# Kernel optimization log

Hardware: AMD Instinct MI355X
Metric: run time of the kernel (lower is better)

## Reference

```python
import jax, jax.numpy as jnp
import numpy as np

D_MODEL = 512
N_HEADS = 8
B, T = 2, 2048
EPS = 1e-6


def _phi(x):
    # ELU feature map: elu(x) + 1 (always positive)
    return jax.nn.elu(x) + 1.0


def setup_inputs() -> dict:
    key = jax.random.key(0)
    ks = jax.random.split(key, 9)
    s = 1.0 / np.sqrt(D_MODEL)
    x = jax.random.normal(ks[0], (B, T, D_MODEL), dtype=jnp.float32)
    Wq = jax.random.uniform(ks[1], (D_MODEL, D_MODEL), jnp.float32, -s, s)
    bq = jax.random.uniform(ks[2], (D_MODEL,), jnp.float32, -s, s)
    Wk = jax.random.uniform(ks[3], (D_MODEL, D_MODEL), jnp.float32, -s, s)
    bk = jax.random.uniform(ks[4], (D_MODEL,), jnp.float32, -s, s)
    Wv = jax.random.uniform(ks[5], (D_MODEL, D_MODEL), jnp.float32, -s, s)
    bv = jax.random.uniform(ks[6], (D_MODEL,), jnp.float32, -s, s)
    Wo = jax.random.uniform(ks[7], (D_MODEL, D_MODEL), jnp.float32, -s, s)
    bo = jax.random.uniform(ks[8], (D_MODEL,), jnp.float32, -s, s)
    return {"x": x, "Wq": Wq, "bq": bq, "Wk": Wk, "bk": bk,
            "Wv": Wv, "bv": bv, "Wo": Wo, "bo": bo}


def reference(x, Wq, bq, Wk, bk, Wv, bv, Wo, bo):
    Bb, Tt, _ = x.shape
    H = N_HEADS
    D = D_MODEL // H

    def heads(W, b):
        # (B,T,d_model) -> (B,H,T,D)
        return (x @ W + b).reshape(Bb, Tt, H, D).transpose(0, 2, 1, 3)

    Q = _phi(heads(Wq, bq))
    K = _phi(heads(Wk, bk))
    V = heads(Wv, bv)

    # Causal linear attention: S_t = sum_{j<=t} phi(K_j) ⊗ V_j, z_t = sum_{j<=t} phi(K_j)
    KV = jnp.einsum('bhtd,bhtm->bhtdm', K, V)   # (B,H,T,D,D)
    S = jnp.cumsum(KV, axis=2)
    z = jnp.cumsum(K, axis=2)
    num = jnp.einsum('bhtd,bhtdm->bhtm', Q, S)  # (B,H,T,D)
    den = jnp.maximum(jnp.einsum('bhtd,bhtd->bht', Q, z), EPS)[..., None]
    out = num / den

    out = out.transpose(0, 2, 1, 3).reshape(Bb, Tt, D_MODEL)
    return out @ Wo + bo
```

## Files before the change

### kernel.cpp

```cpp
#include <hip/hip_runtime.h>
#include <math.h>

#define DM 512
#define NH 8
#define HD 64
#define BB 2
#define TT 2048
#define CHUNK 64
#define NC (TT / CHUNK)
#define BH (BB * NH)
#define ROWS (BB * TT)
#define EPSV 1e-6f

typedef short bf16x8 __attribute__((ext_vector_type(8)));
typedef float f32x4 __attribute__((ext_vector_type(4)));
typedef unsigned short us;

union U4 { us h[4]; uint2 u; };

__device__ __forceinline__ us f2bf(float f) {
    unsigned int u = __float_as_uint(f);
    return (us)((u + 0x7FFFu + ((u >> 16) & 1u)) >> 16);
}
__device__ __forceinline__ float bf2f(us h) {
    return __uint_as_float(((unsigned int)h) << 16);
}
__device__ __forceinline__ void gload16(const void* g, void* l) {
    __builtin_amdgcn_global_load_lds(
        (const __attribute__((address_space(1))) unsigned int*)g,
        (__attribute__((address_space(3))) unsigned int*)l, 16, 0, 0);
}
#define SWZ(r, k) ((k) ^ (((r) & 7) << 3))

__global__ __launch_bounds__(256) void prep(
    const float* __restrict__ x,
    const float* __restrict__ Wq, const float* __restrict__ Wk,
    const float* __restrict__ Wv, const float* __restrict__ Wo,
    us* __restrict__ xb, us* __restrict__ WT)
{
    const int bid = blockIdx.x, tid = threadIdx.x;
    __shared__ float tl[32][33];
    if (bid < 2048) {
        const int i = bid * 256 + tid;
        float4 v = ((const float4*)x)[i];
        U4 o;
        o.h[0] = f2bf(v.x); o.h[1] = f2bf(v.y);
        o.h[2] = f2bf(v.z); o.h[3] = f2bf(v.w);
        ((uint2*)xb)[i] = o.u;
    } else {
        const int b2 = bid - 2048;
        const int which = b2 >> 8, t = b2 & 255;
        const float* W = (which == 0) ? Wq : (which == 1) ? Wk : (which == 2) ? Wv : Wo;
        us* O = WT + (size_t)which * DM * DM;
        const int r0 = (t >> 4) * 32, c0 = (t & 15) * 32;
        const int tr = tid >> 3, tc = tid & 7;
        float4 v = *(const float4*)&W[(size_t)(r0 + tr) * DM + c0 + tc * 4];
        tl[tr][tc * 4 + 0] = v.x; tl[tr][tc * 4 + 1] = v.y;
        tl[tr][tc * 4 + 2] = v.z; tl[tr][tc * 4 + 3] = v.w;
        __syncthreads();
        U4 o;
#pragma unroll
        for (int i = 0; i < 4; ++i) o.h[i] = f2bf(tl[tc * 4 + i][tr]);
        *(uint2*)&O[(size_t)(c0 + tr) * DM + r0 + tc * 4] = o.u;
    }
}

__device__ __forceinline__ void gemm64x128(
    const us* __restrict__ Ag, const us* __restrict__ Bg,
    int r0, int c0, int tid, us* Asl, us* Bsl, f32x4 (&acc)[2][4])
{
    const int lane = tid & 63, wid = tid >> 6;
    const int wr = wid >> 1, wc = wid & 1;
    const int lrow = lane & 15, lk8 = (lane >> 4) * 8;
    const int fa = tid * 8;

    for (int k0 = 0; k0 < DM; k0 += 64) {
        __syncthreads();
#pragma unroll
        for (int i = 0; i < 2; ++i) {
            const int f = fa + i * 2048, row = f >> 6, kp = f & 63;
            gload16(Ag + (size_t)(r0 + row) * DM + k0 + SWZ(row, kp), Asl + f);
        }
#pragma unroll
        for (int i = 0; i < 4; ++i) {
            const int f = fa + i * 2048, row = f >> 6, kp = f & 63;
            gload16(Bg + (size_t)(c0 + row) * DM + k0 + SWZ(row, kp), Bsl + f);
        }
        __syncthreads();
#pragma unroll
        for (int kin = 0; kin < 64; kin += 32) {
            bf16x8 af[2], bfr[4];
#pragma unroll
            for (int mi = 0; mi < 2; ++mi) {
                const int row = wr * 32 + mi * 16 + lrow;
                af[mi] = *(const bf16x8*)&Asl[row * 64 + SWZ(row, kin + lk8)];
            }
#pragma unroll
            for (int ni = 0; ni < 4; ++ni) {
                const int row = wc * 64 + ni * 16 + lrow;
                bfr[ni] = *(const bf16x8*)&Bsl[row * 64 + SWZ(row, kin + lk8)];
            }
#pragma unroll
            for (int mi = 0; mi < 2; ++mi)
#pragma unroll
                for (int ni = 0; ni < 4; ++ni)
                    acc[mi][ni] = __builtin_amdgcn_mfma_f32_16x16x32_bf16(
                        af[mi], bfr[ni], acc[mi][ni], 0, 0, 0);
        }
    }
}

__global__ __launch_bounds__(256) void qkv_mfma(
    const us* __restrict__ xb, const us* __restrict__ WT,
    const float* __restrict__ bq, const float* __restrict__ bk,
    const float* __restrict__ bv,
    us* __restrict__ qn, us* __restrict__ kn,
    us* __restrict__ kt, us* __restrict__ vt)
{
    const int which = blockIdx.z;
    const us* Bg = WT + (size_t)which * DM * DM;
    const float* bias = (which == 0) ? bq : (which == 1) ? bk : bv;

    __shared__ us Asl[64 * 64];
    __shared__ us Bsl[128 * 64];
    f32x4 acc[2][4] = {};
    const int r0 = blockIdx.x * 64, c0 = blockIdx.y * 128;
    const int tid = threadIdx.x;

    gemm64x128(xb, Bg, r0, c0, tid, Asl, Bsl, acc);

    const int lane = tid & 63, wid = tid >> 6;
    const int wr = wid >> 1, wc = wid & 1;
    const int lrow = lane & 15, lr4 = (lane >> 4) * 4;
    const int b = r0 >> 11;

#pragma unroll
    for (int mi = 0; mi < 2; ++mi) {
        const int rowb = r0 + wr * 32 + mi * 16 + lr4;
        const int t0g = rowb & (TT - 1);
#pragma unroll
        for (int ni = 0; ni < 4; ++ni) {
            const int col = c0 + wc * 64 + ni * 16 + lrow;
            const int h = col >> 6, d = col & 63;
            const float bc = bias[col];
            U4 p4;
#pragma unroll
            for (int r = 0; r < 4; ++r) {
                float y = acc[mi][ni][r] + bc;
                if (which < 2) y = (y > 0.f) ? (y + 1.f) : __expf(y);
                const us hb = f2bf(y);
                p4.h[r] = hb;
                if (which == 0)
                    qn[((size_t)(b * NH + h) * TT + t0g + r) * HD + d] = hb;
                else if (which == 1)
                    kn[((size_t)(b * NH + h) * TT + t0g + r) * HD + d] = hb;
            }
            if (which == 1)
                *(uint2*)&kt[((size_t)(b * NH + h) * HD + d) * TT + t0g] = p4.u;
            else if (which == 2)
                *(uint2*)&vt[((size_t)(b * NH + h) * HD + d) * TT + t0g] = p4.u;
        }
    }
}

__global__ __launch_bounds__(256) void out_mfma(
    const us* __restrict__ Ag, const us* __restrict__ WoT,
    const float* __restrict__ bias, float* __restrict__ out)
{
    __shared__ us Asl[64 * 64];
    __shared__ us Bsl[128 * 64];
    f32x4 acc[2][4] = {};
    const int r0 = blockIdx.x * 64, c0 = blockIdx.y * 128;
    const int tid = threadIdx.x;

    gemm64x128(Ag, WoT, r0, c0, tid, Asl, Bsl, acc);

    const int lane = tid & 63, wid = tid >> 6;
    const int wr = wid >> 1, wc = wid & 1;
    const int lrow = lane & 15, lr4 = (lane >> 4) * 4;

#pragma unroll
    for (int mi = 0; mi < 2; ++mi)
#pragma unroll
        for (int ni = 0; ni < 4; ++ni) {
            const int col = c0 + wc * 64 + ni * 16 + lrow;
            const float bc = bias[col];
#pragma unroll
            for (int r = 0; r < 4; ++r) {
                const int row = r0 + wr * 32 + mi * 16 + lr4 + r;
                out[(size_t)row * DM + col] = acc[mi][ni][r] + bc;
            }
        }
}

__global__ __launch_bounds__(256) void chunk_sums(
    const us* __restrict__ kt, const us* __restrict__ vt,
    us* __restrict__ kvc, float* __restrict__ zc)
{
    const int blk = blockIdx.x, bh = blk >> 5, c = blk & 31;
    const int t0 = c * CHUNK;
    __shared__ us Ksl[4096], Vsl[4096];
    __shared__ float partial[4][64];
    const int tid = threadIdx.x;
    const us* ktb = kt + (size_t)bh * HD * TT;
    const us* vtb = vt + (size_t)bh * HD * TT;

#pragma unroll
    for (int i = 0; i < 2; ++i) {
        const int f = tid * 8 + i * 2048, row = f >> 6, kp = f & 63;
        const int kl = SWZ(row, kp);
        gload16(ktb + (size_t)row * TT + t0 + kl, Ksl + f);
        gload16(vtb + (size_t)row * TT + t0 + kl, Vsl + f);
    }
    __syncthreads();

    const int lane = tid & 63, wid = tid >> 6;
    const int wr = wid >> 1, wc = wid & 1;
    const int lrow = lane & 15, lk8 = (lane >> 4) * 8, lr4 = (lane >> 4) * 4;

    f32x4 acc[2][2] = {};
#pragma unroll
    for (int kin = 0; kin < 64; kin += 32) {
        bf16x8 af[2], bfr[2];
#pragma unroll
        for (int mi = 0; mi < 2; ++mi) {
            const int row = wr * 32 + mi * 16 + lrow;
            af[mi] = *(const bf16x8*)&Vsl[row * 64 + SWZ(row, kin + lk8)];
        }
#pragma unroll
        for (int ni = 0; ni < 2; ++ni) {
            const int row = wc * 32 + ni * 16 + lrow;
            bfr[ni] = *(const bf16x8*)&Ksl[row * 64 + SWZ(row, kin + lk8)];
        }
#pragma unroll
        for (int mi = 0; mi < 2; ++mi)
#pragma unroll
            for (int ni = 0; ni < 2; ++ni)
                acc[mi][ni] = __builtin_amdgcn_mfma_f32_16x16x32_bf16(
                    af[mi], bfr[ni], acc[mi][ni], 0, 0, 0);
    }

    us* dst = kvc + (size_t)blk * 4096;
#pragma unroll
    for (int mi = 0; mi < 2; ++mi)
#pragma unroll
        for (int ni = 0; ni < 2; ++ni) {
            const int d2 = wr * 32 + mi * 16 + lr4;
            const int d1 = wc * 32 + ni * 16 + lrow;
#pragma unroll
            for (int r = 0; r < 4; ++r)
                dst[(d2 + r) * 64 + d1] = f2bf(acc[mi][ni][r]);
        }

    {
        const int p = tid >> 6, d = tid & 63;
        float s = 0.f;
#pragma unroll
        for (int j = 0; j < 16; ++j)
            s += bf2f(Ksl[d * 64 + SWZ(d, p * 16 + j)]);
        partial[p][d] = s;
    }
    __syncthreads();
    if (tid < 64)
        zc[(size_t)blk * 64 + tid] =
            partial[0][tid] + partial[1][tid] + partial[2][tid] + partial[3][tid];
}

__global__ __launch_bounds__(256) void scan(
    const us* __restrict__ kvc, const float* __restrict__ zc,
    us* __restrict__ spr, float* __restrict__ zpr)
{
    const int bh = blockIdx.x, seg = blockIdx.y, tid = threadIdx.x;
    if (seg < 8) {
        const int e = seg * 512 + tid * 2;
        float r0 = 0.f, r1 = 0.f;
        for (int c = 0; c < NC; ++c) {
            const size_t off = (size_t)(bh * NC + c) * 4096 + e;
            const unsigned u = *(const unsigned*)(kvc + off);
            const unsigned p = (unsigned)f2bf(r0) | ((unsigned)f2bf(r1) << 16);
            *(unsigned*)(spr + off) = p;
            r0 += bf2f((us)(u & 0xFFFF));
            r1 += bf2f((us)(u >> 16));
        }
    } else if (tid < 64) {
        float run = 0.f;
        for (int c = 0; c < NC; ++c) {
            const size_t off = (size_t)(bh * NC + c) * 64 + tid;
            zpr[off] = run;
            run += zc[off];
        }
    }
}

__global__ __launch_bounds__(256) void chunk_attn(
    const us* __restrict__ qn, const us* __restrict__ kn,
    const us* __restrict__ vt, const us* __restrict__ spr,
    const float* __restrict__ zpr, us* __restrict__ attn)
{
    const int blk = blockIdx.x, bh = blk >> 5, c = blk & 31;
    const int t0 = c * CHUNK;
    __shared__ us Qs[4096], Kns[4096], Vts[4096], Sts[4096], Abf[4096];
    __shared__ float zp[64], den[64], part[4][64];
    const int tid = threadIdx.x;

    const us* qb = qn + ((size_t)bh * TT + t0) * HD;
    const us* kb = kn + ((size_t)bh * TT + t0) * HD;
    const us* vb = vt + (size_t)bh * HD * TT;
    const us* sb = spr + (size_t)blk * 4096;

#pragma unroll
    for (int i = 0; i < 2; ++i) {
        const int f = tid * 8 + i * 2048, row = f >> 6, kp = f & 63;
        const int kl = SWZ(row, kp);
        gload16(qb + (size_t)row * HD + kl, Qs + f);
        gload16(kb + (size_t)row * HD + kl, Kns + f);
        gload16(vb + (size_t)row * TT + t0 + kl, Vts + f);
        gload16(sb + (size_t)row * 64 + kl, Sts + f);
    }
    if (tid < 64) zp[tid] = zpr[(size_t)blk * 64 + tid];
    __syncthreads();

    const int lane = tid & 63, wid = tid >> 6;
    const int wr = wid >> 1, wc = wid & 1;
    const int lrow = lane & 15, lk8 = (lane >> 4) * 8, lr4 = (lane >> 4) * 4;

    f32x4 accs[2][2] = {};
#pragma unroll
    for (int kin = 0; kin < 64; kin += 32) {
        bf16x8 af[2], bfr[2];
#pragma unroll
        for (int mi = 0; mi < 2; ++mi) {
            const int row = wr * 32 + mi * 16 + lrow;
            af[mi] = *(const bf16x8*)&Qs[row * 64 + SWZ(row, kin + lk8)];
        }
#pragma unroll
        for (int ni = 0; ni < 2; ++ni) {
            const int row = wc * 32 + ni * 16 + lrow;
            bfr[ni] = *(const bf16x8*)&Kns[row * 64 + SWZ(row, kin + lk8)];
        }
#pragma unroll
        for (int mi = 0; mi < 2; ++mi)
#pragma unroll
            for (int ni = 0; ni < 2; ++ni)
                accs[mi][ni] = __builtin_amdgcn_mfma_f32_16x16x32_bf16(
                    af[mi], bfr[ni], accs[mi][ni], 0, 0, 0);
    }

#pragma unroll
    for (int mi = 0; mi < 2; ++mi)
#pragma unroll
        for (int ni = 0; ni < 2; ++ni) {
            const int j = wc * 32 + ni * 16 + lrow;
#pragma unroll
            for (int r = 0; r < 4; ++r) {
                const int i = wr * 32 + mi * 16 + lr4 + r;
                const float v = (j <= i) ? accs[mi][ni][r] : 0.f;
                Abf[i * 64 + SWZ(i, j)] = f2bf(v);
            }
        }
    __syncthreads();

    {
        const int p = tid >> 6, i = tid & 63;
        float s = 0.f;
#pragma unroll
        for (int jj = 0; jj < 16; ++jj) {
            const int j = p * 16 + jj;
            s += bf2f(Abf[i * 64 + SWZ(i, j)]);
            s += bf2f(Qs[i * 64 + SWZ(i, j)]) * zp[j];
        }
        part[p][i] = s;
    }
    __syncthreads();
    if (tid < 64)
        den[tid] = fmaxf(part[0][tid] + part[1][tid] + part[2][tid] + part[3][tid], EPSV);
    __syncthreads();

    f32x4 acco[2][2] = {};
#pragma unroll
    for (int kin = 0; kin < 64; kin += 32) {
        bf16x8 af[2], bfr[2], ag[2], bgr[2];
#pragma unroll
        for (int mi = 0; mi < 2; ++mi) {
            const int row = wr * 32 + mi * 16 + lrow;
            af[mi] = *(const bf16x8*)&Abf[row * 64 + SWZ(row, kin + lk8)];
            ag[mi] = *(const bf16x8*)&Qs[row * 64 + SWZ(row, kin + lk8)];
        }
#pragma unroll
        for (int ni = 0; ni < 2; ++ni) {
            const int row = wc * 32 + ni * 16 + lrow;
            bfr[ni] = *(const bf16x8*)&Vts[row * 64 + SWZ(row, kin + lk8)];
            bgr[ni] = *(const bf16x8*)&Sts[row * 64 + SWZ(row, kin + lk8)];
        }
#pragma unroll
        for (int mi = 0; mi < 2; ++mi)
#pragma unroll
            for (int ni = 0; ni < 2; ++ni) {
                acco[mi][ni] = __builtin_amdgcn_mfma_f32_16x16x32_bf16(
                    af[mi], bfr[ni], acco[mi][ni], 0, 0, 0);
                acco[mi][ni] = __builtin_amdgcn_mfma_f32_16x16x32_bf16(
                    ag[mi], bgr[ni], acco[mi][ni], 0, 0, 0);
            }
    }

    const int b = bh >> 3, h = bh & 7;
#pragma unroll
    for (int mi = 0; mi < 2; ++mi)
#pragma unroll
        for (int ni = 0; ni < 2; ++ni) {
            const int d2 = wc * 32 + ni * 16 + lrow;
#pragma unroll
            for (int r = 0; r < 4; ++r) {
                const int i = wr * 32 + mi * 16 + lr4 + r;
                attn[((size_t)b * TT + t0 + i) * DM + h * HD + d2] =
                    f2bf(acco[mi][ni][r] / den[i]);
            }
        }
}

extern "C" void kernel_launch(void* const* d_in, const int* in_sizes, int n_in,
                              void* d_out, int out_size, void* d_ws, size_t ws_size,
                              hipStream_t stream)
{
    const float* x  = (const float*)d_in[0];
    const float* Wq = (const float*)d_in[1];
    const float* bq = (const float*)d_in[2];
    const float* Wk = (const float*)d_in[3];
    const float* bk = (const float*)d_in[4];
    const float* Wv = (const float*)d_in[5];
    const float* bv = (const float*)d_in[6];
    const float* Wo = (const float*)d_in[7];
    const float* bo = (const float*)d_in[8];
    float* out = (float*)d_out;

    const size_t SZ = (size_t)BH * TT * HD;
    us* xb  = (us*)d_ws;
    us* WT  = xb + SZ;
    us* qn  = WT + (size_t)4 * DM * DM;
    us* kn  = qn + SZ;
    us* kt  = kn + SZ;
    us* vt  = kt + SZ;
    us* kvc = vt + SZ;
    us* spr = kvc + SZ;
    float* zc  = (float*)(spr + SZ);
    float* zpr = zc + (size_t)BH * NC * 64;
    us* attn = xb;

    prep<<<3072, 256, 0, stream>>>(x, Wq, Wk, Wv, Wo, xb, WT);
    qkv_mfma<<<dim3(ROWS / 64, DM / 128, 3), 256, 0, stream>>>(
        xb, WT, bq, bk, bv, qn, kn, kt, vt);
    chunk_sums<<<BH * NC, 256, 0, stream>>>(kt, vt, kvc, zc);
    scan<<<dim3(BH, 9), 256, 0, stream>>>(kvc, zc, spr, zpr);
    chunk_attn<<<BH * NC, 256, 0, stream>>>(qn, kn, vt, spr, zpr, attn);
    out_mfma<<<dim3(ROWS / 64, DM / 128), 256, 0, stream>>>(attn, WT + (size_t)3 * DM * DM, bo, out);
}
```

Baseline: 48.39 us.

## Double-buffer GEMM tiles and restructure chunk kernels to per-wave strips with MFMA reductions

The shared GEMM helper now double-buffers its LDS tiles, loading the next K slice while computing the current one, and keeps one barrier per step. chunk_sums and chunk_attn are rewritten so each wave owns a 16-row strip and reads operands straight from global memory instead of staging through LDS. Their scalar reduction loops for the key sums and the denominator are replaced with MFMAs against a ones/z vector. This removes LDS staging and several block barriers. In exchange it doubles GEMM LDS use, which may lower occupancy, and relies on uncoalesced direct global fragment loads.

```diff
diff --git a/kernel.cpp b/kernel.cpp
--- a/kernel.cpp
+++ b/kernel.cpp
@@ -65,6 +65,23 @@
     }
 }
 
+__device__ __forceinline__ void stage_tiles(
+    const us* __restrict__ Ag, const us* __restrict__ Bg,
+    int r0, int c0, int k0, int tid, us* As, us* Bs)
+{
+    const int fa = tid * 8;
+#pragma unroll
+    for (int i = 0; i < 2; ++i) {
+        const int f = fa + i * 2048, row = f >> 6, kp = f & 63;
+        gload16(Ag + (size_t)(r0 + row) * DM + k0 + SWZ(row, kp), As + f);
+    }
+#pragma unroll
+    for (int i = 0; i < 4; ++i) {
+        const int f = fa + i * 2048, row = f >> 6, kp = f & 63;
+        gload16(Bg + (size_t)(c0 + row) * DM + k0 + SWZ(row, kp), Bs + f);
+    }
+}
+
 __device__ __forceinline__ void gemm64x128(
     const us* __restrict__ Ag, const us* __restrict__ Bg,
     int r0, int c0, int tid, us* Asl, us* Bsl, f32x4 (&acc)[2][4])
@@ -72,33 +89,28 @@
     const int lane = tid & 63, wid = tid >> 6;
     const int wr = wid >> 1, wc = wid & 1;
     const int lrow = lane & 15, lk8 = (lane >> 4) * 8;
-    const int fa = tid * 8;
-
+
+    stage_tiles(Ag, Bg, r0, c0, 0, tid, Asl, Bsl);
+    __syncthreads();
+    int cur = 0;
     for (int k0 = 0; k0 < DM; k0 += 64) {
-        __syncthreads();
-#pragma unroll
-        for (int i = 0; i < 2; ++i) {
-            const int f = fa + i * 2048, row = f >> 6, kp = f & 63;
-            gload16(Ag + (size_t)(r0 + row) * DM + k0 + SWZ(row, kp), Asl + f);
-        }
-#pragma unroll
-        for (int i = 0; i < 4; ++i) {
-            const int f = fa + i * 2048, row = f >> 6, kp = f & 63;
-            gload16(Bg + (size_t)(c0 + row) * DM + k0 + SWZ(row, kp), Bsl + f);
-        }
-        __syncthreads();
+        if (k0 + 64 < DM)
+            stage_tiles(Ag, Bg, r0, c0, k0 + 64, tid,
+                        Asl + (cur ^ 1) * 4096, Bsl + (cur ^ 1) * 8192);
+        const us* As = Asl + cur * 4096;
+        const us* Bs = Bsl + cur * 8192;
 #pragma unroll
         for (int kin = 0; kin < 64; kin += 32) {
             bf16x8 af[2], bfr[4];
 #pragma unroll
             for (int mi = 0; mi < 2; ++mi) {
                 const int row = wr * 32 + mi * 16 + lrow;
-                af[mi] = *(const bf16x8*)&Asl[row * 64 + SWZ(row, kin + lk8)];
+                af[mi] = *(const bf16x8*)&As[row * 64 + SWZ(row, kin + lk8)];
             }
 #pragma unroll
             for (int ni = 0; ni < 4; ++ni) {
                 const int row = wc * 64 + ni * 16 + lrow;
-                bfr[ni] = *(const bf16x8*)&Bsl[row * 64 + SWZ(row, kin + lk8)];
+                bfr[ni] = *(const bf16x8*)&Bs[row * 64 + SWZ(row, kin + lk8)];
             }
 #pragma unroll
             for (int mi = 0; mi < 2; ++mi)
@@ -107,6 +119,8 @@
                     acc[mi][ni] = __builtin_amdgcn_mfma_f32_16x16x32_bf16(
                         af[mi], bfr[ni], acc[mi][ni], 0, 0, 0);
         }
+        __syncthreads();
+        cur ^= 1;
     }
 }
 
@@ -121,8 +135,8 @@
     const us* Bg = WT + (size_t)which * DM * DM;
     const float* bias = (which == 0) ? bq : (which == 1) ? bk : bv;
 
-    __shared__ us Asl[64 * 64];
-    __shared__ us Bsl[128 * 64];
+    __shared__ us Asl[2 * 4096];
+    __shared__ us Bsl[2 * 8192];
     f32x4 acc[2][4] = {};
     const int r0 = blockIdx.x * 64, c0 = blockIdx.y * 128;
     const int tid = threadIdx.x;
@@ -167,8 +181,8 @@
     const us* __restrict__ Ag, const us* __restrict__ WoT,
     const float* __restrict__ bias, float* __restrict__ out)
 {
-    __shared__ us Asl[64 * 64];
-    __shared__ us Bsl[128 * 64];
+    __shared__ us Asl[2 * 4096];
+    __shared__ us Bsl[2 * 8192];
     f32x4 acc[2][4] = {};
     const int r0 = blockIdx.x * 64, c0 = blockIdx.y * 128;
     const int tid = threadIdx.x;
@@ -199,71 +213,47 @@
 {
     const int blk = blockIdx.x, bh = blk >> 5, c = blk & 31;
     const int t0 = c * CHUNK;
-    __shared__ us Ksl[4096], Vsl[4096];
-    __shared__ float partial[4][64];
-    const int tid = threadIdx.x;
-    const us* ktb = kt + (size_t)bh * HD * TT;
-    const us* vtb = vt + (size_t)bh * HD * TT;
-
-#pragma unroll
-    for (int i = 0; i < 2; ++i) {
-        const int f = tid * 8 + i * 2048, row = f >> 6, kp = f & 63;
-        const int kl = SWZ(row, kp);
-        gload16(ktb + (size_t)row * TT + t0 + kl, Ksl + f);
-        gload16(vtb + (size_t)row * TT + t0 + kl, Vsl + f);
-    }
-    __syncthreads();
-
-    const int lane = tid & 63, wid = tid >> 6;
-    const int wr = wid >> 1, wc = wid & 1;
+    const int tid = threadIdx.x, lane = tid & 63, wid = tid >> 6;
+    const int strip = wid * 16;
     const int lrow = lane & 15, lk8 = (lane >> 4) * 8, lr4 = (lane >> 4) * 4;
 
-    f32x4 acc[2][2] = {};
+    const us* ktb = kt + (size_t)bh * HD * TT + t0;
+    const us* vtb = vt + (size_t)bh * HD * TT + t0;
+
+    bf16x8 onesf = {};
+    if (lrow == 0)
+#pragma unroll
+        for (int e = 0; e < 8; ++e) onesf[e] = (short)0x3F80;
+
+    f32x4 acc[4] = {};
+    f32x4 accz[4] = {};
 #pragma unroll
     for (int kin = 0; kin < 64; kin += 32) {
-        bf16x8 af[2], bfr[2];
-#pragma unroll
-        for (int mi = 0; mi < 2; ++mi) {
-            const int row = wr * 32 + mi * 16 + lrow;
-            af[mi] = *(const bf16x8*)&Vsl[row * 64 + SWZ(row, kin + lk8)];
-        }
-#pragma unroll
-        for (int ni = 0; ni < 2; ++ni) {
-            const int row = wc * 32 + ni * 16 + lrow;
-            bfr[ni] = *(const bf16x8*)&Ksl[row * 64 + SWZ(row, kin + lk8)];
-        }
-#pragma unroll
-        for (int mi = 0; mi < 2; ++mi)
-#pragma unroll
-            for (int ni = 0; ni < 2; ++ni)
-                acc[mi][ni] = __builtin_amdgcn_mfma_f32_16x16x32_bf16(
-                    af[mi], bfr[ni], acc[mi][ni], 0, 0, 0);
+        const bf16x8 av = *(const bf16x8*)&vtb[(size_t)(strip + lrow) * TT + kin + lk8];
+        bf16x8 bk[4];
+#pragma unroll
+        for (int nj = 0; nj < 4; ++nj)
+            bk[nj] = *(const bf16x8*)&ktb[(size_t)(nj * 16 + lrow) * TT + kin + lk8];
+#pragma unroll
+        for (int nj = 0; nj < 4; ++nj)
+            acc[nj] = __builtin_amdgcn_mfma_f32_16x16x32_bf16(av, bk[nj], acc[nj], 0, 0, 0);
+        if (wid == 3)
+#pragma unroll
+            for (int nj = 0; nj < 4; ++nj)
+                accz[nj] = __builtin_amdgcn_mfma_f32_16x16x32_bf16(onesf, bk[nj], accz[nj], 0, 0, 0);
     }
 
     us* dst = kvc + (size_t)blk * 4096;
 #pragma unroll
-    for (int mi = 0; mi < 2; ++mi)
-#pragma unroll
-        for (int ni = 0; ni < 2; ++ni) {
-            const int d2 = wr * 32 + mi * 16 + lr4;
-            const int d1 = wc * 32 + ni * 16 + lrow;
-#pragma unroll
-            for (int r = 0; r < 4; ++r)
-                dst[(d2 + r) * 64 + d1] = f2bf(acc[mi][ni][r]);
-        }
-
-    {
-        const int p = tid >> 6, d = tid & 63;
-        float s = 0.f;
-#pragma unroll
-        for (int j = 0; j < 16; ++j)
-            s += bf2f(Ksl[d * 64 + SWZ(d, p * 16 + j)]);
-        partial[p][d] = s;
-    }
-    __syncthreads();
-    if (tid < 64)
-        zc[(size_t)blk * 64 + tid] =
-            partial[0][tid] + partial[1][tid] + partial[2][tid] + partial[3][tid];
+    for (int nj = 0; nj < 4; ++nj)
+#pragma unroll
+        for (int r = 0; r < 4; ++r)
+            dst[(strip + lr4 + r) * 64 + nj * 16 + lrow] = f2bf(acc[nj][r]);
+
+    if (wid == 3 && lane < 16)
+#pragma unroll
+        for (int nj = 0; nj < 4; ++nj)
+            zc[(size_t)blk * 64 + nj * 16 + lane] = accz[nj][0];
 }
 
 __global__ __launch_bounds__(256) void scan(
@@ -299,122 +289,90 @@
 {
     const int blk = blockIdx.x, bh = blk >> 5, c = blk & 31;
     const int t0 = c * CHUNK;
-    __shared__ us Qs[4096], Kns[4096], Vts[4096], Sts[4096], Abf[4096];
-    __shared__ float zp[64], den[64], part[4][64];
-    const int tid = threadIdx.x;
+    const int tid = threadIdx.x, lane = tid & 63, wid = tid >> 6;
+    const int strip = wid * 16;
+    const int lrow = lane & 15, lk8 = (lane >> 4) * 8, lr4 = (lane >> 4) * 4;
+
+    __shared__ us Abf[4][1024];
 
     const us* qb = qn + ((size_t)bh * TT + t0) * HD;
     const us* kb = kn + ((size_t)bh * TT + t0) * HD;
-    const us* vb = vt + (size_t)bh * HD * TT;
+    const us* vb = vt + (size_t)bh * HD * TT + t0;
     const us* sb = spr + (size_t)blk * 4096;
-
-#pragma unroll
-    for (int i = 0; i < 2; ++i) {
-        const int f = tid * 8 + i * 2048, row = f >> 6, kp = f & 63;
-        const int kl = SWZ(row, kp);
-        gload16(qb + (size_t)row * HD + kl, Qs + f);
-        gload16(kb + (size_t)row * HD + kl, Kns + f);
-        gload16(vb + (size_t)row * TT + t0 + kl, Vts + f);
-        gload16(sb + (size_t)row * 64 + kl, Sts + f);
-    }
-    if (tid < 64) zp[tid] = zpr[(size_t)blk * 64 + tid];
-    __syncthreads();
-
-    const int lane = tid & 63, wid = tid >> 6;
-    const int wr = wid >> 1, wc = wid & 1;
-    const int lrow = lane & 15, lk8 = (lane >> 4) * 8, lr4 = (lane >> 4) * 4;
-
-    f32x4 accs[2][2] = {};
-#pragma unroll
-    for (int kin = 0; kin < 64; kin += 32) {
-        bf16x8 af[2], bfr[2];
-#pragma unroll
-        for (int mi = 0; mi < 2; ++mi) {
-            const int row = wr * 32 + mi * 16 + lrow;
-            af[mi] = *(const bf16x8*)&Qs[row * 64 + SWZ(row, kin + lk8)];
-        }
-#pragma unroll
-        for (int ni = 0; ni < 2; ++ni) {
-            const int row = wc * 32 + ni * 16 + lrow;
-            bfr[ni] = *(const bf16x8*)&Kns[row * 64 + SWZ(row, kin + lk8)];
-        }
-#pragma unroll
-        for (int mi = 0; mi < 2; ++mi)
-#pragma unroll
-            for (int ni = 0; ni < 2; ++ni)
-                accs[mi][ni] = __builtin_amdgcn_mfma_f32_16x16x32_bf16(
-                    af[mi], bfr[ni], accs[mi][ni], 0, 0, 0);
-    }
-
-#pragma unroll
-    for (int mi = 0; mi < 2; ++mi)
-#pragma unroll
-        for (int ni = 0; ni < 2; ++ni) {
-            const int j = wc * 32 + ni * 16 + lrow;
-#pragma unroll
-            for (int r = 0; r < 4; ++r) {
-                const int i = wr * 32 + mi * 16 + lr4 + r;
-                const float v = (j <= i) ? accs[mi][ni][r] : 0.f;
-                Abf[i * 64 + SWZ(i, j)] = f2bf(v);
-            }
-        }
-    __syncthreads();
-
-    {
-        const int p = tid >> 6, i = tid & 63;
-        float s = 0.f;
-#pragma unroll
-        for (int jj = 0; jj < 16; ++jj) {
-            const int j = p * 16 + jj;
-            s += bf2f(Abf[i * 64 + SWZ(i, j)]);
-            s += bf2f(Qs[i * 64 + SWZ(i, j)]) * zp[j];
-        }
-        part[p][i] = s;
-    }
-    __syncthreads();
-    if (tid < 64)
-        den[tid] = fmaxf(part[0][tid] + part[1][tid] + part[2][tid] + part[3][tid], EPSV);
-    __syncthreads();
-
-    f32x4 acco[2][2] = {};
-#pragma unroll
-    for (int kin = 0; kin < 64; kin += 32) {
-        bf16x8 af[2], bfr[2], ag[2], bgr[2];
-#pragma unroll
-        for (int mi = 0; mi < 2; ++mi) {
-            const int row = wr * 32 + mi * 16 + lrow;
-            af[mi] = *(const bf16x8*)&Abf[row * 64 + SWZ(row, kin + lk8)];
-            ag[mi] = *(const bf16x8*)&Qs[row * 64 + SWZ(row, kin + lk8)];
-        }
-#pragma unroll
-        for (int ni = 0; ni < 2; ++ni) {
-            const int row = wc * 32 + ni * 16 + lrow;
-            bfr[ni] = *(const bf16x8*)&Vts[row * 64 + SWZ(row, kin + lk8)];
-            bgr[ni] = *(const bf16x8*)&Sts[row * 64 + SWZ(row, kin + lk8)];
-        }
-#pragma unroll
-        for (int mi = 0; mi < 2; ++mi)
-#pragma unroll
-            for (int ni = 0; ni < 2; ++ni) {
-                acco[mi][ni] = __builtin_amdgcn_mfma_f32_16x16x32_bf16(
-                    af[mi], bfr[ni], acco[mi][ni], 0, 0, 0);
-                acco[mi][ni] = __builtin_amdgcn_mfma_f32_16x16x32_bf16(
-                    ag[mi], bgr[ni], acco[mi][ni], 0, 0, 0);
-            }
-    }
+    const float* zb = zpr + (size_t)blk * 64;
+
+    bf16x8 af_q[2];
+#pragma unroll
+    for (int kin = 0; kin < 2; ++kin)
+        af_q[kin] = *(const bf16x8*)&qb[(size_t)(strip + lrow) * HD + kin * 32 + lk8];
+
+    f32x4 accs[4] = {};
+#pragma unroll
+    for (int kin = 0; kin < 2; ++kin)
+#pragma unroll
+        for (int nj = 0; nj < 4; ++nj) {
+            const bf16x8 bk = *(const bf16x8*)&kb[(size_t)(nj * 16 + lrow) * HD + kin * 32 + lk8];
+            accs[nj] = __builtin_amdgcn_mfma_f32_16x16x32_bf16(af_q[kin], bk, accs[nj], 0, 0, 0);
+        }
+
+#pragma unroll
+    for (int nj = 0; nj < 4; ++nj)
+#pragma unroll
+        for (int r = 0; r < 4; ++r) {
+            const int il = lr4 + r, j = nj * 16 + lrow;
+            Abf[wid][il * 64 + SWZ(il, j)] =
+                (j <= strip + il) ? f2bf(accs[nj][r]) : (us)0;
+        }
+
+    bf16x8 af_a[2];
+#pragma unroll
+    for (int kin = 0; kin < 2; ++kin)
+        af_a[kin] = *(const bf16x8*)&Abf[wid][lrow * 64 + SWZ(lrow, kin * 32 + lk8)];
+
+    bf16x8 onesf = {}, zf[2];
+#pragma unroll
+    for (int kin = 0; kin < 2; ++kin) {
+        bf16x8 z8 = {};
+        const float4 za = *(const float4*)&zb[kin * 32 + lk8];
+        const float4 zb4 = *(const float4*)&zb[kin * 32 + lk8 + 4];
+        z8[0] = (short)f2bf(za.x); z8[1] = (short)f2bf(za.y);
+        z8[2] = (short)f2bf(za.z); z8[3] = (short)f2bf(za.w);
+        z8[4] = (short)f2bf(zb4.x); z8[5] = (short)f2bf(zb4.y);
+        z8[6] = (short)f2bf(zb4.z); z8[7] = (short)f2bf(zb4.w);
+        zf[kin] = (lrow == 0) ? z8 : (bf16x8){};
+    }
+    if (lrow == 0)
+#pragma unroll
+        for (int e = 0; e < 8; ++e) onesf[e] = (short)0x3F80;
+
+    f32x4 acco[4] = {};
+    f32x4 accd = {};
+#pragma unroll
+    for (int kin = 0; kin < 2; ++kin) {
+        accd = __builtin_amdgcn_mfma_f32_16x16x32_bf16(af_a[kin], onesf, accd, 0, 0, 0);
+        accd = __builtin_amdgcn_mfma_f32_16x16x32_bf16(af_q[kin], zf[kin], accd, 0, 0, 0);
+#pragma unroll
+        for (int nd = 0; nd < 4; ++nd) {
+            const bf16x8 bv = *(const bf16x8*)&vb[(size_t)(nd * 16 + lrow) * TT + kin * 32 + lk8];
+            const bf16x8 bs = *(const bf16x8*)&sb[(size_t)(nd * 16 + lrow) * 64 + kin * 32 + lk8];
+            acco[nd] = __builtin_amdgcn_mfma_f32_16x16x32_bf16(af_a[kin], bv, acco[nd], 0, 0, 0);
+            acco[nd] = __builtin_amdgcn_mfma_f32_16x16x32_bf16(af_q[kin], bs, acco[nd], 0, 0, 0);
+        }
+    }
+
+    float denr[4];
+#pragma unroll
+    for (int r = 0; r < 4; ++r)
+        denr[r] = fmaxf(__shfl(accd[r], (int)(lane & 48), 64), EPSV);
 
     const int b = bh >> 3, h = bh & 7;
 #pragma unroll
-    for (int mi = 0; mi < 2; ++mi)
-#pragma unroll
-        for (int ni = 0; ni < 2; ++ni) {
-            const int d2 = wc * 32 + ni * 16 + lrow;
-#pragma unroll
-            for (int r = 0; r < 4; ++r) {
-                const int i = wr * 32 + mi * 16 + lr4 + r;
-                attn[((size_t)b * TT + t0 + i) * DM + h * HD + d2] =
-                    f2bf(acco[mi][ni][r] / den[i]);
-            }
+    for (int nd = 0; nd < 4; ++nd)
+#pragma unroll
+        for (int r = 0; r < 4; ++r) {
+            const int i = t0 + strip + lr4 + r;
+            const int d2 = nd * 16 + lrow;
+            attn[((size_t)b * TT + i) * DM + h * HD + d2] = f2bf(acco[nd][r] / denr[r]);
         }
 }
 
@@ -452,5 +410,6 @@
     chunk_sums<<<BH * NC, 256, 0, stream>>>(kt, vt, kvc, zc);
     scan<<<dim3(BH, 9), 256, 0, stream>>>(kvc, zc, spr, zpr);
     chunk_attn<<<BH * NC, 256, 0, stream>>>(qn, kn, vt, spr, zpr, attn);
-    out_mfma<<<dim3(ROWS / 64, DM / 128), 256, 0, stream>>>(attn, WT + (size_t)3 * DM * DM, bo, out);
-}
+    out_mfma<<<dim3(ROWS / 64, DM / 128), 256, 0, stream>>>(
+        attn, WT + (size_t)3 * DM * DM, bo, out);
+}
```

Measured after the change: 54.93 us. 13.5% more time.

## Fuse x conversion into QKV GEMM, replace scan with segmented prefix sums

Applied to the files above, without the earlier changes.

The separate fp32-to-bf16 conversion of x is removed: the QKV GEMM now loads fp32 x and converts it while staging into LDS. The chunk-sum and serial scan kernels are replaced by one kernel. It keeps running KV and z state over 4-chunk segments, using an MFMA with a ones vector for the z sums. chunk_attn then adds earlier segment totals itself, and computes the denominator with extra MFMAs against ones and z vectors instead of a shared-memory reduction. Together this drops two launches and several intermediate buffers. In exchange the x loads become non-async, chunk_attn does redundant segment-sum work, and bf16 rounding is applied to z for the denominator MFMA.

```diff
diff --git a/kernel.cpp b/kernel.cpp
--- a/kernel.cpp
+++ b/kernel.cpp
@@ -17,6 +17,7 @@
 typedef unsigned short us;
 
 union U4 { us h[4]; uint2 u; };
+union U8 { us h[8]; uint4 u; };
 
 __device__ __forceinline__ us f2bf(float f) {
     unsigned int u = __float_as_uint(f);
@@ -32,43 +33,46 @@
 }
 #define SWZ(r, k) ((k) ^ (((r) & 7) << 3))
 
-__global__ __launch_bounds__(256) void prep(
-    const float* __restrict__ x,
+__global__ __launch_bounds__(256) void prepW(
     const float* __restrict__ Wq, const float* __restrict__ Wk,
     const float* __restrict__ Wv, const float* __restrict__ Wo,
-    us* __restrict__ xb, us* __restrict__ WT)
+    us* __restrict__ WT)
 {
     const int bid = blockIdx.x, tid = threadIdx.x;
+    const int which = bid >> 8, t = bid & 255;
+    const float* W = (which == 0) ? Wq : (which == 1) ? Wk : (which == 2) ? Wv : Wo;
+    us* O = WT + (size_t)which * DM * DM;
+
     __shared__ float tl[32][33];
-    if (bid < 2048) {
-        const int i = bid * 256 + tid;
-        float4 v = ((const float4*)x)[i];
-        U4 o;
-        o.h[0] = f2bf(v.x); o.h[1] = f2bf(v.y);
-        o.h[2] = f2bf(v.z); o.h[3] = f2bf(v.w);
-        ((uint2*)xb)[i] = o.u;
-    } else {
-        const int b2 = bid - 2048;
-        const int which = b2 >> 8, t = b2 & 255;
-        const float* W = (which == 0) ? Wq : (which == 1) ? Wk : (which == 2) ? Wv : Wo;
-        us* O = WT + (size_t)which * DM * DM;
-        const int r0 = (t >> 4) * 32, c0 = (t & 15) * 32;
-        const int tr = tid >> 3, tc = tid & 7;
-        float4 v = *(const float4*)&W[(size_t)(r0 + tr) * DM + c0 + tc * 4];
-        tl[tr][tc * 4 + 0] = v.x; tl[tr][tc * 4 + 1] = v.y;
-        tl[tr][tc * 4 + 2] = v.z; tl[tr][tc * 4 + 3] = v.w;
-        __syncthreads();
-        U4 o;
-#pragma unroll
-        for (int i = 0; i < 4; ++i) o.h[i] = f2bf(tl[tc * 4 + i][tr]);
-        *(uint2*)&O[(size_t)(c0 + tr) * DM + r0 + tc * 4] = o.u;
-    }
-}
-
-__device__ __forceinline__ void gemm64x128(
-    const us* __restrict__ Ag, const us* __restrict__ Bg,
-    int r0, int c0, int tid, us* Asl, us* Bsl, f32x4 (&acc)[2][4])
-{
+    const int r0 = (t >> 4) * 32, c0 = (t & 15) * 32;
+    const int tr = tid >> 3, tc = tid & 7;
+    float4 v = *(const float4*)&W[(size_t)(r0 + tr) * DM + c0 + tc * 4];
+    tl[tr][tc * 4 + 0] = v.x; tl[tr][tc * 4 + 1] = v.y;
+    tl[tr][tc * 4 + 2] = v.z; tl[tr][tc * 4 + 3] = v.w;
+    __syncthreads();
+    U4 o;
+#pragma unroll
+    for (int i = 0; i < 4; ++i) o.h[i] = f2bf(tl[tc * 4 + i][tr]);
+    *(uint2*)&O[(size_t)(c0 + tr) * DM + r0 + tc * 4] = o.u;
+}
+
+__global__ __launch_bounds__(256) void qkv_mfma(
+    const float* __restrict__ x, const us* __restrict__ WT,
+    const float* __restrict__ bq, const float* __restrict__ bk,
+    const float* __restrict__ bv,
+    us* __restrict__ qn, us* __restrict__ kn,
+    us* __restrict__ kt, us* __restrict__ vt)
+{
+    const int which = blockIdx.z;
+    const us* Bg = WT + (size_t)which * DM * DM;
+    const float* bias = (which == 0) ? bq : (which == 1) ? bk : bv;
+
+    __shared__ us Asl[4096];
+    __shared__ us Bsl[8192];
+
+    f32x4 acc[2][4] = {};
+    const int r0 = blockIdx.x * 64, c0 = blockIdx.y * 128;
+    const int tid = threadIdx.x;
     const int lane = tid & 63, wid = tid >> 6;
     const int wr = wid >> 1, wc = wid & 1;
     const int lrow = lane & 15, lk8 = (lane >> 4) * 8;
@@ -79,7 +83,14 @@
 #pragma unroll
         for (int i = 0; i < 2; ++i) {
             const int f = fa + i * 2048, row = f >> 6, kp = f & 63;
-            gload16(Ag + (size_t)(r0 + row) * DM + k0 + SWZ(row, kp), Asl + f);
+            const float4 xa = *(const float4*)&x[(size_t)(r0 + row) * DM + k0 + kp];
+            const float4 xc = *(const float4*)&x[(size_t)(r0 + row) * DM + k0 + kp + 4];
+            U8 p;
+            p.h[0] = f2bf(xa.x); p.h[1] = f2bf(xa.y);
+            p.h[2] = f2bf(xa.z); p.h[3] = f2bf(xa.w);
+            p.h[4] = f2bf(xc.x); p.h[5] = f2bf(xc.y);
+            p.h[6] = f2bf(xc.z); p.h[7] = f2bf(xc.w);
+            *(uint4*)&Asl[row * 64 + SWZ(row, kp)] = p.u;
         }
 #pragma unroll
         for (int i = 0; i < 4; ++i) {
@@ -108,30 +119,8 @@
                         af[mi], bfr[ni], acc[mi][ni], 0, 0, 0);
         }
     }
-}
-
-__global__ __launch_bounds__(256) void qkv_mfma(
-    const us* __restrict__ xb, const us* __restrict__ WT,
-    const float* __restrict__ bq, const float* __restrict__ bk,
-    const float* __restrict__ bv,
-    us* __restrict__ qn, us* __restrict__ kn,
-    us* __restrict__ kt, us* __restrict__ vt)
-{
-    const int which = blockIdx.z;
-    const us* Bg = WT + (size_t)which * DM * DM;
-    const float* bias = (which == 0) ? bq : (which == 1) ? bk : bv;
-
-    __shared__ us Asl[64 * 64];
-    __shared__ us Bsl[128 * 64];
-    f32x4 acc[2][4] = {};
-    const int r0 = blockIdx.x * 64, c0 = blockIdx.y * 128;
-    const int tid = threadIdx.x;
-
-    gemm64x128(xb, Bg, r0, c0, tid, Asl, Bsl, acc);
-
-    const int lane = tid & 63, wid = tid >> 6;
-    const int wr = wid >> 1, wc = wid & 1;
-    const int lrow = lane & 15, lr4 = (lane >> 4) * 4;
+
+    const int lr4 = (lane >> 4) * 4;
     const int b = r0 >> 11;
 
 #pragma unroll
@@ -167,18 +156,52 @@
     const us* __restrict__ Ag, const us* __restrict__ WoT,
     const float* __restrict__ bias, float* __restrict__ out)
 {
-    __shared__ us Asl[64 * 64];
-    __shared__ us Bsl[128 * 64];
+    __shared__ us Asl[4096];
+    __shared__ us Bsl[8192];
     f32x4 acc[2][4] = {};
     const int r0 = blockIdx.x * 64, c0 = blockIdx.y * 128;
     const int tid = threadIdx.x;
-
-    gemm64x128(Ag, WoT, r0, c0, tid, Asl, Bsl, acc);
-
     const int lane = tid & 63, wid = tid >> 6;
     const int wr = wid >> 1, wc = wid & 1;
-    const int lrow = lane & 15, lr4 = (lane >> 4) * 4;
-
+    const int lrow = lane & 15, lk8 = (lane >> 4) * 8;
+    const int fa = tid * 8;
+
+    for (int k0 = 0; k0 < DM; k0 += 64) {
+        __syncthreads();
+#pragma unroll
+        for (int i = 0; i < 2; ++i) {
+            const int f = fa + i * 2048, row = f >> 6, kp = f & 63;
+            gload16(Ag + (size_t)(r0 + row) * DM + k0 + SWZ(row, kp), Asl + f);
+        }
+#pragma unroll
+        for (int i = 0; i < 4; ++i) {
+            const int f = fa + i * 2048, row = f >> 6, kp = f & 63;
+            gload16(WoT + (size_t)(c0 + row) * DM + k0 + SWZ(row, kp), Bsl + f);
+        }
+        __syncthreads();
+#pragma unroll
+        for (int kin = 0; kin < 64; kin += 32) {
+            bf16x8 af[2], bfr[4];
+#pragma unroll
+            for (int mi = 0; mi < 2; ++mi) {
+                const int row = wr * 32 + mi * 16 + lrow;
+                af[mi] = *(const bf16x8*)&Asl[row * 64 + SWZ(row, kin + lk8)];
+            }
+#pragma unroll
+            for (int ni = 0; ni < 4; ++ni) {
+                const int row = wc * 64 + ni * 16 + lrow;
+                bfr[ni] = *(const bf16x8*)&Bsl[row * 64 + SWZ(row, kin + lk8)];
+            }
+#pragma unroll
+            for (int mi = 0; mi < 2; ++mi)
+#pragma unroll
+                for (int ni = 0; ni < 4; ++ni)
+                    acc[mi][ni] = __builtin_amdgcn_mfma_f32_16x16x32_bf16(
+                        af[mi], bfr[ni], acc[mi][ni], 0, 0, 0);
+        }
+    }
+
+    const int lr4 = (lane >> 4) * 4;
 #pragma unroll
     for (int mi = 0; mi < 2; ++mi)
 #pragma unroll
@@ -193,54 +216,82 @@
         }
 }
 
-__global__ __launch_bounds__(256) void chunk_sums(
+__global__ __launch_bounds__(256) void sums_seg(
     const us* __restrict__ kt, const us* __restrict__ vt,
-    us* __restrict__ kvc, float* __restrict__ zc)
-{
-    const int blk = blockIdx.x, bh = blk >> 5, c = blk & 31;
-    const int t0 = c * CHUNK;
+    us* __restrict__ spr, us* __restrict__ segsum,
+    float* __restrict__ zloc, float* __restrict__ zseg)
+{
+    const int bid = blockIdx.x;
+    const int bh = bid >> 3, seg = bid & 7;
     __shared__ us Ksl[4096], Vsl[4096];
-    __shared__ float partial[4][64];
-    const int tid = threadIdx.x;
+    const int tid = threadIdx.x, lane = tid & 63, wid = tid >> 6;
+    const int wr = wid >> 1, wc = wid & 1;
+    const int lrow = lane & 15, lk8 = (lane >> 4) * 8, lr4 = (lane >> 4) * 4;
     const us* ktb = kt + (size_t)bh * HD * TT;
     const us* vtb = vt + (size_t)bh * HD * TT;
 
-#pragma unroll
-    for (int i = 0; i < 2; ++i) {
-        const int f = tid * 8 + i * 2048, row = f >> 6, kp = f & 63;
-        const int kl = SWZ(row, kp);
-        gload16(ktb + (size_t)row * TT + t0 + kl, Ksl + f);
-        gload16(vtb + (size_t)row * TT + t0 + kl, Vsl + f);
-    }
-    __syncthreads();
-
-    const int lane = tid & 63, wid = tid >> 6;
-    const int wr = wid >> 1, wc = wid & 1;
-    const int lrow = lane & 15, lk8 = (lane >> 4) * 8, lr4 = (lane >> 4) * 4;
-
-    f32x4 acc[2][2] = {};
-#pragma unroll
-    for (int kin = 0; kin < 64; kin += 32) {
-        bf16x8 af[2], bfr[2];
-#pragma unroll
-        for (int mi = 0; mi < 2; ++mi) {
-            const int row = wr * 32 + mi * 16 + lrow;
-            af[mi] = *(const bf16x8*)&Vsl[row * 64 + SWZ(row, kin + lk8)];
-        }
-#pragma unroll
-        for (int ni = 0; ni < 2; ++ni) {
-            const int row = wc * 32 + ni * 16 + lrow;
-            bfr[ni] = *(const bf16x8*)&Ksl[row * 64 + SWZ(row, kin + lk8)];
-        }
+    bf16x8 onesA = {};
+    if (lrow == 0)
+#pragma unroll
+        for (int e = 0; e < 8; ++e) onesA[e] = (short)0x3F80;
+
+    f32x4 run[2][2] = {};
+    f32x4 runz[2] = {};
+
+    for (int cc = 0; cc < 4; ++cc) {
+        const int c = seg * 4 + cc, t0 = c * CHUNK;
+        __syncthreads();
+#pragma unroll
+        for (int i = 0; i < 2; ++i) {
+            const int f = tid * 8 + i * 2048, row = f >> 6, kp = f & 63;
+            const int kl = SWZ(row, kp);
+            gload16(ktb + (size_t)row * TT + t0 + kl, Ksl + f);
+            gload16(vtb + (size_t)row * TT + t0 + kl, Vsl + f);
+        }
+        us* dst = spr + (size_t)(bh * NC + c) * 4096;
 #pragma unroll
         for (int mi = 0; mi < 2; ++mi)
 #pragma unroll
+            for (int ni = 0; ni < 2; ++ni) {
+                const int d2 = wr * 32 + mi * 16 + lr4;
+                const int d1 = wc * 32 + ni * 16 + lrow;
+#pragma unroll
+                for (int r = 0; r < 4; ++r)
+                    dst[(d2 + r) * 64 + d1] = f2bf(run[mi][ni][r]);
+            }
+        if (wr == 0 && lane < 16)
+#pragma unroll
             for (int ni = 0; ni < 2; ++ni)
-                acc[mi][ni] = __builtin_amdgcn_mfma_f32_16x16x32_bf16(
-                    af[mi], bfr[ni], acc[mi][ni], 0, 0, 0);
-    }
-
-    us* dst = kvc + (size_t)blk * 4096;
+                zloc[(size_t)(bh * NC + c) * 64 + wc * 32 + ni * 16 + lane] = runz[ni][0];
+        __syncthreads();
+#pragma unroll
+        for (int kin = 0; kin < 64; kin += 32) {
+            bf16x8 af[2], bfr[2];
+#pragma unroll
+            for (int mi = 0; mi < 2; ++mi) {
+                const int row = wr * 32 + mi * 16 + lrow;
+                af[mi] = *(const bf16x8*)&Vsl[row * 64 + SWZ(row, kin + lk8)];
+            }
+#pragma unroll
+            for (int ni = 0; ni < 2; ++ni) {
+                const int row = wc * 32 + ni * 16 + lrow;
+                bfr[ni] = *(const bf16x8*)&Ksl[row * 64 + SWZ(row, kin + lk8)];
+            }
+#pragma unroll
+            for (int mi = 0; mi < 2; ++mi)
+#pragma unroll
+                for (int ni = 0; ni < 2; ++ni)
+                    run[mi][ni] = __builtin_amdgcn_mfma_f32_16x16x32_bf16(
+                        af[mi], bfr[ni], run[mi][ni], 0, 0, 0);
+            if (wr == 0)
+#pragma unroll
+                for (int ni = 0; ni < 2; ++ni)
+                    runz[ni] = __builtin_amdgcn_mfma_f32_16x16x32_bf16(
+                        onesA, bfr[ni], runz[ni], 0, 0, 0);
+        }
+    }
+
+    us* sdst = segsum + (size_t)(bh * 8 + seg) * 4096;
 #pragma unroll
     for (int mi = 0; mi < 2; ++mi)
 #pragma unroll
@@ -249,64 +300,31 @@
             const int d1 = wc * 32 + ni * 16 + lrow;
 #pragma unroll
             for (int r = 0; r < 4; ++r)
-                dst[(d2 + r) * 64 + d1] = f2bf(acc[mi][ni][r]);
-        }
-
-    {
-        const int p = tid >> 6, d = tid & 63;
-        float s = 0.f;
-#pragma unroll
-        for (int j = 0; j < 16; ++j)
-            s += bf2f(Ksl[d * 64 + SWZ(d, p * 16 + j)]);
-        partial[p][d] = s;
-    }
-    __syncthreads();
-    if (tid < 64)
-        zc[(size_t)blk * 64 + tid] =
-            partial[0][tid] + partial[1][tid] + partial[2][tid] + partial[3][tid];
-}
-
-__global__ __launch_bounds__(256) void scan(
-    const us* __restrict__ kvc, const float* __restrict__ zc,
-    us* __restrict__ spr, float* __restrict__ zpr)
-{
-    const int bh = blockIdx.x, seg = blockIdx.y, tid = threadIdx.x;
-    if (seg < 8) {
-        const int e = seg * 512 + tid * 2;
-        float r0 = 0.f, r1 = 0.f;
-        for (int c = 0; c < NC; ++c) {
-            const size_t off = (size_t)(bh * NC + c) * 4096 + e;
-            const unsigned u = *(const unsigned*)(kvc + off);
-            const unsigned p = (unsigned)f2bf(r0) | ((unsigned)f2bf(r1) << 16);
-            *(unsigned*)(spr + off) = p;
-            r0 += bf2f((us)(u & 0xFFFF));
-            r1 += bf2f((us)(u >> 16));
-        }
-    } else if (tid < 64) {
-        float run = 0.f;
-        for (int c = 0; c < NC; ++c) {
-            const size_t off = (size_t)(bh * NC + c) * 64 + tid;
-            zpr[off] = run;
-            run += zc[off];
-        }
-    }
+                sdst[(d2 + r) * 64 + d1] = f2bf(run[mi][ni][r]);
+        }
+    if (wr == 0 && lane < 16)
+#pragma unroll
+        for (int ni = 0; ni < 2; ++ni)
+            zseg[(size_t)(bh * 8 + seg) * 64 + wc * 32 + ni * 16 + lane] = runz[ni][0];
 }
 
 __global__ __launch_bounds__(256) void chunk_attn(
     const us* __restrict__ qn, const us* __restrict__ kn,
     const us* __restrict__ vt, const us* __restrict__ spr,
-    const float* __restrict__ zpr, us* __restrict__ attn)
+    const us* __restrict__ segsum, const float* __restrict__ zloc,
+    const float* __restrict__ zseg, us* __restrict__ attn)
 {
     const int blk = blockIdx.x, bh = blk >> 5, c = blk & 31;
-    const int t0 = c * CHUNK;
+    const int t0 = c * CHUNK, seg = c >> 2;
     __shared__ us Qs[4096], Kns[4096], Vts[4096], Sts[4096], Abf[4096];
-    __shared__ float zp[64], den[64], part[4][64];
+    __shared__ float zp[64];
     const int tid = threadIdx.x;
 
     const us* qb = qn + ((size_t)bh * TT + t0) * HD;
     const us* kb = kn + ((size_t)bh * TT + t0) * HD;
     const us* vb = vt + (size_t)bh * HD * TT;
-    const us* sb = spr + (size_t)blk * 4096;
+    const us* sprL = spr + (size_t)blk * 4096;
+    const us* segb = segsum + (size_t)(bh * 8) * 4096;
 
 #pragma unroll
     for (int i = 0; i < 2; ++i) {
@@ -315,9 +333,29 @@
         gload16(qb + (size_t)row * HD + kl, Qs + f);
         gload16(kb + (size_t)row * HD + kl, Kns + f);
         gload16(vb + (size_t)row * TT + t0 + kl, Vts + f);
-        gload16(sb + (size_t)row * 64 + kl, Sts + f);
-    }
-    if (tid < 64) zp[tid] = zpr[(size_t)blk * 64 + tid];
+    }
+#pragma unroll
+    for (int i = 0; i < 2; ++i) {
+        const int f = tid * 8 + i * 2048, row = f >> 6, kp = f & 63;
+        float sacc[8];
+        const bf16x8 v0 = *(const bf16x8*)&sprL[row * 64 + kp];
+#pragma unroll
+        for (int e = 0; e < 8; ++e) sacc[e] = bf2f((us)v0[e]);
+        for (int s = 0; s < seg; ++s) {
+            const bf16x8 vs = *(const bf16x8*)&segb[(size_t)s * 4096 + row * 64 + kp];
+#pragma unroll
+            for (int e = 0; e < 8; ++e) sacc[e] += bf2f((us)vs[e]);
+        }
+        U8 p;
+#pragma unroll
+        for (int e = 0; e < 8; ++e) p.h[e] = f2bf(sacc[e]);
+        *(uint4*)&Sts[row * 64 + SWZ(row, kp)] = p.u;
+    }
+    if (tid < 64) {
+        float zv = zloc[(size_t)blk * 64 + tid];
+        for (int s = 0; s < seg; ++s) zv += zseg[(size_t)(bh * 8 + s) * 64 + tid];
+        zp[tid] = zv;
+    }
     __syncthreads();
 
     const int lane = tid & 63, wid = tid >> 6;
@@ -360,31 +398,25 @@
         }
     __syncthreads();
 
-    {
-        const int p = tid >> 6, i = tid & 63;
-        float s = 0.f;
-#pragma unroll
-        for (int jj = 0; jj < 16; ++jj) {
-            const int j = p * 16 + jj;
-            s += bf2f(Abf[i * 64 + SWZ(i, j)]);
-            s += bf2f(Qs[i * 64 + SWZ(i, j)]) * zp[j];
-        }
-        part[p][i] = s;
-    }
-    __syncthreads();
-    if (tid < 64)
-        den[tid] = fmaxf(part[0][tid] + part[1][tid] + part[2][tid] + part[3][tid], EPSV);
-    __syncthreads();
+    bf16x8 onesB = {}, zB = {};
+    if (lrow == 0) {
+#pragma unroll
+        for (int e = 0; e < 8; ++e) {
+            onesB[e] = (short)0x3F80;
+            zB[e] = (short)f2bf(zp[lk8 + e]);
+        }
+    }
 
     f32x4 acco[2][2] = {};
+    f32x4 accd[2] = {};
 #pragma unroll
     for (int kin = 0; kin < 64; kin += 32) {
-        bf16x8 af[2], bfr[2], ag[2], bgr[2];
+        bf16x8 af_a[2], af_q[2], bfr[2], bgr[2];
 #pragma unroll
         for (int mi = 0; mi < 2; ++mi) {
             const int row = wr * 32 + mi * 16 + lrow;
-            af[mi] = *(const bf16x8*)&Abf[row * 64 + SWZ(row, kin + lk8)];
-            ag[mi] = *(const bf16x8*)&Qs[row * 64 + SWZ(row, kin + lk8)];
+            af_a[mi] = *(const bf16x8*)&Abf[row * 64 + SWZ(row, kin + lk8)];
+            af_q[mi] = *(const bf16x8*)&Qs[row * 64 + SWZ(row, kin + lk8)];
         }
 #pragma unroll
         for (int ni = 0; ni < 2; ++ni) {
@@ -393,15 +425,27 @@
             bgr[ni] = *(const bf16x8*)&Sts[row * 64 + SWZ(row, kin + lk8)];
         }
 #pragma unroll
-        for (int mi = 0; mi < 2; ++mi)
+        for (int mi = 0; mi < 2; ++mi) {
+            accd[mi] = __builtin_amdgcn_mfma_f32_16x16x32_bf16(
+                af_a[mi], onesB, accd[mi], 0, 0, 0);
+            accd[mi] = __builtin_amdgcn_mfma_f32_16x16x32_bf16(
+                af_q[mi], zB, accd[mi], 0, 0, 0);
 #pragma unroll
             for (int ni = 0; ni < 2; ++ni) {
                 acco[mi][ni] = __builtin_amdgcn_mfma_f32_16x16x32_bf16(
-                    af[mi], bfr[ni], acco[mi][ni], 0, 0, 0);
+                    af_a[mi], bfr[ni], acco[mi][ni], 0, 0, 0);
                 acco[mi][ni] = __builtin_amdgcn_mfma_f32_16x16x32_bf16(
-                    ag[mi], bgr[ni], acco[mi][ni], 0, 0, 0);
-            }
-    }
+                    af_q[mi], bgr[ni], acco[mi][ni], 0, 0, 0);
+            }
+        }
+    }
+
+    float denr[2][4];
+#pragma unroll
+    for (int mi = 0; mi < 2; ++mi)
+#pragma unroll
+        for (int r = 0; r < 4; ++r)
+            denr[mi][r] = fmaxf(__shfl(accd[mi][r], (int)(lane & 48), 64), EPSV);
 
     const int b = bh >> 3, h = bh & 7;
 #pragma unroll
@@ -413,7 +457,7 @@
             for (int r = 0; r < 4; ++r) {
                 const int i = wr * 32 + mi * 16 + lr4 + r;
                 attn[((size_t)b * TT + t0 + i) * DM + h * HD + d2] =
-                    f2bf(acco[mi][ni][r] / den[i]);
+                    f2bf(acco[mi][ni][r] / denr[mi][r]);
             }
         }
 }
@@ -434,23 +478,22 @@
     float* out = (float*)d_out;
 
     const size_t SZ = (size_t)BH * TT * HD;
-    us* xb  = (us*)d_ws;
-    us* WT  = xb + SZ;
-    us* qn  = WT + (size_t)4 * DM * DM;
-    us* kn  = qn + SZ;
-    us* kt  = kn + SZ;
-    us* vt  = kt + SZ;
-    us* kvc = vt + SZ;
-    us* spr = kvc + SZ;
-    float* zc  = (float*)(spr + SZ);
-    float* zpr = zc + (size_t)BH * NC * 64;
-    us* attn = xb;
-
-    prep<<<3072, 256, 0, stream>>>(x, Wq, Wk, Wv, Wo, xb, WT);
+    us* WT   = (us*)d_ws;
+    us* qn   = WT + (size_t)4 * DM * DM;
+    us* kn   = qn + SZ;
+    us* kt   = kn + SZ;
+    us* vt   = kt + SZ;
+    us* spr  = vt + SZ;
+    us* segsum = spr + SZ;
+    us* attn = segsum + (size_t)BH * 8 * 4096;
+    float* zloc = (float*)(attn + SZ);
+    float* zseg = zloc + (size_t)BH * NC * 64;
+
+    prepW<<<1024, 256, 0, stream>>>(Wq, Wk, Wv, Wo, WT);
     qkv_mfma<<<dim3(ROWS / 64, DM / 128, 3), 256, 0, stream>>>(
-        xb, WT, bq, bk, bv, qn, kn, kt, vt);
-    chunk_sums<<<BH * NC, 256, 0, stream>>>(kt, vt, kvc, zc);
-    scan<<<dim3(BH, 9), 256, 0, stream>>>(kvc, zc, spr, zpr);
-    chunk_attn<<<BH * NC, 256, 0, stream>>>(qn, kn, vt, spr, zpr, attn);
-    out_mfma<<<dim3(ROWS / 64, DM / 128), 256, 0, stream>>>(attn, WT + (size_t)3 * DM * DM, bo, out);
-}
+        x, WT, bq, bk, bv, qn, kn, kt, vt);
+    sums_seg<<<BH * 8, 256, 0, stream>>>(kt, vt, spr, segsum, zloc, zseg);
+    chunk_attn<<<BH * NC, 256, 0, stream>>>(qn, kn, vt, spr, segsum, zloc, zseg, attn);
+    out_mfma<<<dim3(ROWS / 64, DM / 128), 256, 0, stream>>>(
+        attn, WT + (size_t)3 * DM * DM, bo, out);
+}
```

Measured after the change: 52.63 us. 1.09x slower.
